# Optimization experiments

Measured on AMD Instinct MI355X. Metric: run time of the kernel, lower is better.

## Reference

```python
import jax, jax.numpy as jnp
import numpy as np
import math

H = 2048; NH = 16; HD = 128; E = 8; K = 2; F = 8192; CAP_F = 1.25
B = 2; S = 2048

def _layernorm(x, scale, bias, eps=1e-5):
    m = jnp.mean(x, axis=-1, keepdims=True)
    v = jnp.var(x, axis=-1, keepdims=True)
    return (x - m) * jax.lax.rsqrt(v + eps) * scale + bias

def _rope(x):
    # x: [B, S, NH, HD]; half-split RoPE, theta=10000
    hd = x.shape[-1]
    pos = jnp.arange(x.shape[1], dtype=jnp.float32)
    freqs = 1.0 / (10000.0 ** (jnp.arange(0, hd // 2, dtype=jnp.float32) / (hd // 2)))
    ang = pos[:, None] * freqs[None, :]              # [S, HD/2]
    cos = jnp.cos(ang)[None, :, None, :]
    sin = jnp.sin(ang)[None, :, None, :]
    x1, x2 = jnp.split(x, 2, axis=-1)
    return jnp.concatenate([x1 * cos - x2 * sin, x1 * sin + x2 * cos], axis=-1)

def setup_inputs() -> dict:
    key = jax.random.key(0)
    ks = jax.random.split(key, 16)
    std = 0.02
    inp = {
        'hidden_states': jax.random.normal(ks[0], (B, S, H), jnp.float32),
        'attention_mask': jnp.ones((B, S), jnp.int32),
        'ln1_scale': jnp.ones((H,), jnp.float32), 'ln1_bias': jnp.zeros((H,), jnp.float32),
        'ln2_scale': jnp.ones((H,), jnp.float32), 'ln2_bias': jnp.zeros((H,), jnp.float32),
        'Wq': jax.random.normal(ks[1], (H, NH * HD), jnp.float32) * std,
        'Wk': jax.random.normal(ks[2], (H, NH * HD), jnp.float32) * std,
        'Wv': jax.random.normal(ks[3], (H, NH * HD), jnp.float32) * std,
        'Wo': jax.random.normal(ks[4], (NH * HD, H), jnp.float32) * std,
        'Wg': jax.random.normal(ks[5], (H, H), jnp.float32) * std,
        'bg': jnp.zeros((H,), jnp.float32),
        'ls_attn': jnp.full((H,), 0.1, jnp.float32),
        'ls_moe': jnp.full((H,), 0.1, jnp.float32),
        'router_w': jax.random.normal(ks[6], (H, E), jnp.float32) * std,
        'W1': jax.random.normal(ks[7], (E, H, F), jnp.float32) * std,
        'b1': jnp.zeros((E, F), jnp.float32),
        'W2': jax.random.normal(ks[8], (E, F, H), jnp.float32) * std,
        'b2': jnp.zeros((E, H), jnp.float32),
    }
    return inp

def _forward(hidden_states, attention_mask, ln1_scale, ln1_bias, ln2_scale, ln2_bias,
             Wq, Wk, Wv, Wo, Wg, bg, ls_attn, ls_moe, router_w, W1, b1, W2, b2):
    b, s, h = hidden_states.shape
    # ---- pre-norm MLA attention + residual ----
    xn = _layernorm(hidden_states, ln1_scale, ln1_bias)
    q = (xn @ Wq).reshape(b, s, NH, HD)
    k = (xn @ Wk).reshape(b, s, NH, HD)
    v = (xn @ Wv).reshape(b, s, NH, HD)
    q = _rope(q); k = _rope(k)
    scores = jnp.einsum('bqhd,bkhd->bhqk', q, k) / math.sqrt(HD)
    causal = jnp.tril(jnp.ones((s, s), bool))
    mask = causal[None, None, :, :] & (attention_mask[:, None, None, :] > 0)
    scores = jnp.where(mask, scores, -1e9)
    attn = jax.nn.softmax(scores, axis=-1)
    ctx = jnp.einsum('bhqk,bkhd->bqhd', attn, v).reshape(b, s, NH * HD)
    attn_out = ctx @ Wo
    attn_out = attn_out * jax.nn.sigmoid(xn @ Wg + bg)   # output gating
    attn_out = attn_out * ls_attn                         # layer scale
    hidden_states = hidden_states + attn_out
    # ---- pre-norm MoE FFN + residual ----
    xn2 = _layernorm(hidden_states, ln2_scale, ln2_bias)
    T = b * s
    x = xn2.reshape(T, h)
    logits = (x @ router_w).astype(jnp.float32)           # [T, E]
    probs = jax.nn.softmax(logits, axis=-1)
    gates, idx = jax.lax.top_k(probs, K)                  # [T, K]
    gates = gates / jnp.sum(gates, axis=-1, keepdims=True)
    cap = int(math.ceil(T * K / E * CAP_F))               # expert capacity
    e_flat = idx.reshape(T * K)
    g_flat = gates.reshape(T * K)
    oh = jax.nn.one_hot(e_flat, E, dtype=jnp.int32)       # [TK, E]
    pos = jnp.sum(jnp.cumsum(oh, axis=0) * oh, axis=-1) - 1
    keep = (pos < cap).astype(x.dtype)
    pos_c = jnp.clip(pos, 0, cap - 1)
    x_rep = jnp.repeat(x, K, axis=0)                      # [TK, H]
    buf = jnp.zeros((E, cap, h), x.dtype).at[e_flat, pos_c].add(x_rep * keep[:, None])
    hmid = jax.nn.gelu(jnp.einsum('ech,ehf->ecf', buf, W1) + b1[:, None, :])
    obuf = jnp.einsum('ecf,efh->ech', hmid, W2) + b2[:, None, :]
    tok = obuf[e_flat, pos_c] * (keep * g_flat)[:, None]  # [TK, H]
    moe_out = tok.reshape(T, K, h).sum(axis=1).reshape(b, s, h)
    moe_out = moe_out * ls_moe
    return hidden_states + moe_out

def reference(hidden_states, attention_mask, ln1_scale, ln1_bias, ln2_scale, ln2_bias,
              Wq, Wk, Wv, Wo, Wg, bg, ls_attn, ls_moe, router_w, W1, b1, W2, b2):
    return _forward(hidden_states, attention_mask, ln1_scale, ln1_bias, ln2_scale, ln2_bias,
                    Wq, Wk, Wv, Wo, Wg, bg, ls_attn, ls_moe, router_w, W1, b1, W2, b2)
```

## Files before the change

kernel.cpp:

```cpp
#include <hip/hip_runtime.h>
#include <hip/hip_fp16.h>

typedef _Float16 f16;
typedef _Float16 half4 __attribute__((ext_vector_type(4)));
typedef _Float16 half8 __attribute__((ext_vector_type(8)));
typedef float floatx4 __attribute__((ext_vector_type(4)));

constexpr int kH  = 2048;
constexpr int kS  = 2048;
constexpr int kB  = 2;
constexpr int kT  = kB * kS;
constexpr int kNH = 16;
constexpr int kHD = 128;
constexpr int kE  = 8;
constexpr int kF  = 8192;
constexpr int kCAP = 1280;
constexpr int kTK = kT * 2;

__device__ __forceinline__ void gload16(const void* g, void* lds_) {
  __builtin_amdgcn_global_load_lds((const __attribute__((address_space(1))) void*)g,
                                   (__attribute__((address_space(3))) void*)lds_,
                                   16, 0, 0);
}

__device__ __forceinline__ void xcd_remap(int& bx, int& by, int& bz) {
  const int gx = gridDim.x, gy = gridDim.y;
  const int nwg = gx * gy * gridDim.z;
  int L = (bz * gy + by) * gx + bx;
  L = (L & 7) * (nwg >> 3) + (L >> 3);
  bz = L / (gx * gy);
  const int r = L - bz * gx * gy;
  by = r / gx;  bx = r - by * gx;
}

__global__ __launch_bounds__(256) void transpose_cvt(
    const float* __restrict__ src, f16* __restrict__ dst,
    int ldS, int ldD, long sZ, long dZ)
{
  __shared__ float tile[64][65];
  src += (long)blockIdx.z * sZ;
  dst += (long)blockIdx.z * dZ;
  const int kb = blockIdx.y * 64, nb = blockIdx.x * 64;
  const int tx = threadIdx.x & 15, ty = threadIdx.x >> 4;
#pragma unroll
  for (int i = 0; i < 4; i++) {
    const int r = ty + i * 16;
    const float4 v = *(const float4*)&src[(long)(kb + r) * ldS + nb + tx * 4];
    tile[r][tx * 4 + 0] = v.x; tile[r][tx * 4 + 1] = v.y;
    tile[r][tx * 4 + 2] = v.z; tile[r][tx * 4 + 3] = v.w;
  }
  __syncthreads();
  const int tx8 = threadIdx.x & 7, ty32 = threadIdx.x >> 3;
#pragma unroll
  for (int i = 0; i < 2; i++) {
    const int n = ty32 + i * 32;
    union { f16 h[8]; float4 v; } pk;
#pragma unroll
    for (int j = 0; j < 8; j++) pk.h[j] = (f16)tile[tx8 * 8 + j][n];
    *(float4*)&dst[(long)(nb + n) * ldD + kb + tx8 * 8] = pk.v;
  }
}

__global__ __launch_bounds__(256) void transpose_cvt5(
    const float* __restrict__ s0, const float* __restrict__ s1,
    const float* __restrict__ s2, const float* __restrict__ s3,
    const float* __restrict__ s4, f16* __restrict__ dst)
{
  __shared__ float tile[64][65];
  const float* src;
  switch (blockIdx.z) {
    case 0: src = s0; break;
    case 1: src = s1; break;
    case 2: src = s2; break;
    case 3: src = s3; break;
    default: src = s4; break;
  }
  dst += (long)blockIdx.z * kH * kH;
  const int kb = blockIdx.y * 64, nb = blockIdx.x * 64;
  const int tx = threadIdx.x & 15, ty = threadIdx.x >> 4;
#pragma unroll
  for (int i = 0; i < 4; i++) {
    const int r = ty + i * 16;
    const float4 v = *(const float4*)&src[(long)(kb + r) * kH + nb + tx * 4];
    tile[r][tx * 4 + 0] = v.x; tile[r][tx * 4 + 1] = v.y;
    tile[r][tx * 4 + 2] = v.z; tile[r][tx * 4 + 3] = v.w;
  }
  __syncthreads();
  const int tx8 = threadIdx.x & 7, ty32 = threadIdx.x >> 3;
#pragma unroll
  for (int i = 0; i < 2; i++) {
    const int n = ty32 + i * 32;
    union { f16 h[8]; float4 v; } pk;
#pragma unroll
    for (int j = 0; j < 8; j++) pk.h[j] = (f16)tile[tx8 * 8 + j][n];
    *(float4*)&dst[(long)(nb + n) * kH + kb + tx8 * 8] = pk.v;
  }
}

__global__ __launch_bounds__(256) void transpose_f16(
    const f16* __restrict__ src, f16* __restrict__ dst,
    int ldS, int ldD, long sZ, long dZ)
{
  __shared__ f16 tile[64][80];
  src += (long)blockIdx.z * sZ;
  dst += (long)blockIdx.z * dZ;
  const int kb = blockIdx.y * 64, nb = blockIdx.x * 64;
  const int tx = threadIdx.x & 7, ty = threadIdx.x >> 3;
#pragma unroll
  for (int i = 0; i < 2; i++) {
    const int r = ty + i * 32;
    *(half8*)&tile[r][tx * 8] =
        *(const half8*)&src[(long)(kb + r) * ldS + nb + tx * 8];
  }
  __syncthreads();
#pragma unroll
  for (int i = 0; i < 2; i++) {
    const int n = ty + i * 32;
    union { f16 h[8]; float4 v; } pk;
#pragma unroll
    for (int j = 0; j < 8; j++) pk.h[j] = tile[tx * 8 + j][n];
    *(float4*)&dst[(long)(nb + n) * ldD + kb + tx * 8] = pk.v;
  }
}

__global__ __launch_bounds__(256) void ln_kernel(
    const float* __restrict__ x, const float* __restrict__ sc,
    const float* __restrict__ bi, f16* __restrict__ o16, float* __restrict__ o32)
{
  const long row = blockIdx.x;
  const float* xr = x + row * kH;
  const int t = threadIdx.x;
  const float4 u = ((const float4*)xr)[t * 2];
  const float4 v = ((const float4*)xr)[t * 2 + 1];
  float s = u.x + u.y + u.z + u.w + v.x + v.y + v.z + v.w;
  float q = u.x*u.x + u.y*u.y + u.z*u.z + u.w*u.w + v.x*v.x + v.y*v.y + v.z*v.z + v.w*v.w;
#pragma unroll
  for (int m = 1; m < 64; m <<= 1) { s += __shfl_xor(s, m); q += __shfl_xor(q, m); }
  __shared__ float red_s[4], red_q[4];
  const int w = t >> 6, l = t & 63;
  if (l == 0) { red_s[w] = s; red_q[w] = q; }
  __syncthreads();
  s = red_s[0] + red_s[1] + red_s[2] + red_s[3];
  q = red_q[0] + red_q[1] + red_q[2] + red_q[3];
  const float mean = s * (1.f / kH);
  const float var = q * (1.f / kH) - mean * mean;
  const float rstd = rsqrtf(var + 1e-5f);
  const int c = t * 8;
  const float vals[8] = {u.x, u.y, u.z, u.w, v.x, v.y, v.z, v.w};
#pragma unroll
  for (int j = 0; j < 8; j++) {
    const float y = (vals[j] - mean) * rstd * sc[c + j] + bi[c + j];
    o16[row * kH + c + j] = (f16)y;
    if (o32 != nullptr) o32[row * kH + c + j] = y;
  }
}

#define STG(SRC, TILE, KC, PAR, MAT) { \
  const f16* s_ = (SRC) + (long)(TILE) * 64 + (KC) * 32; \
  char* d_ = lds + ((PAR) * 65536 + (MAT) * 32768 + (KC) * 16384) + ldsW; \
  gload16(s_, d_); \
  gload16(s_ + 128 * ldGl, d_ + 8192); }

#define MROW(MH, MM, AF) \
  acc[(MH)*4+(MM)][0] = __builtin_amdgcn_mfma_f32_16x16x32_f16(AF, bf0, acc[(MH)*4+(MM)][0], 0, 0, 0); \
  acc[(MH)*4+(MM)][1] = __builtin_amdgcn_mfma_f32_16x16x32_f16(AF, bf1, acc[(MH)*4+(MM)][1], 0, 0, 0); \
  acc[(MH)*4+(MM)][2] = __builtin_amdgcn_mfma_f32_16x16x32_f16(AF, bf2, acc[(MH)*4+(MM)][2], 0, 0, 0); \
  acc[(MH)*4+(MM)][3] = __builtin_amdgcn_mfma_f32_16x16x32_f16(AF, bf3, acc[(MH)*4+(MM)][3], 0, 0, 0);

#define PH(PAR, KC, MH, RB, STAGE_STMT, VM_STMT) { \
  const char* au_ = lds + ((PAR) * 65536 + (KC) * 16384); \
  const char* bu_ = lds + ((PAR) * 65536 + 32768 + (KC) * 16384); \
  af0 = *(const half8*)(au_ + afoff + (MH) * 4096 +    0); \
  af1 = *(const half8*)(au_ + afoff + (MH) * 4096 + 1024); \
  af2 = *(const half8*)(au_ + afoff + (MH) * 4096 + 2048); \
  af3 = *(const half8*)(au_ + afoff + (MH) * 4096 + 3072); \
  if (RB) { \
    bf0 = *(const half8*)(bu_ + bfoff +    0); \
    bf1 = *(const half8*)(bu_ + bfoff + 1024); \
    bf2 = *(const half8*)(bu_ + bfoff + 2048); \
    bf3 = *(const half8*)(bu_ + bfoff + 3072); \
  } \
  STAGE_STMT; \
  VM_STMT; \
  __builtin_amdgcn_sched_barrier(0); \
  __builtin_amdgcn_s_barrier(); \
  asm volatile("s_waitcnt lgkmcnt(0)" ::: "memory"); \
  __builtin_amdgcn_sched_barrier(0); \
  __builtin_amdgcn_s_setprio(1); \
  MROW(MH, 0, af0) MROW(MH, 1, af1) MROW(MH, 2, af2) MROW(MH, 3, af3) \
  __builtin_amdgcn_s_setprio(0); }

#define VM10 asm volatile("s_waitcnt vmcnt(10)" ::: "memory")
#define VM8  asm volatile("s_waitcnt vmcnt(8)" ::: "memory")
#define VM4  asm volatile("s_waitcnt vmcnt(4)" ::: "memory")
#define VM0  asm volatile("s_waitcnt vmcnt(0)" ::: "memory")
#define NOP (void)0

template <int EPI, int SK, bool XCD>
__global__ __launch_bounds__(512, 2) void gemm8p_kernel(
    const f16* __restrict__ A, const f16* __restrict__ B, void* __restrict__ Cv,
    const float* __restrict__ bias, const int* __restrict__ rowCount,
    int M, int N, int K, long ldA, long ldB, long aZ, long bZ, long cZ,
    long cZ2, long biasZ)
{
  int bx = blockIdx.x, by = blockIdx.y, bz = blockIdx.z;
  if (XCD) xcd_remap(bx, by, bz);
  const int z = bz;
  const int ze = z / SK;
  const int kq = z % SK;
  if (rowCount != nullptr && (int)(by * 256) >= rowCount[ze]) return;
  __shared__ __align__(16) char lds[131072];
  const long khoff = (long)kq * K;
  A += (long)ze * aZ + khoff;  B += (long)ze * bZ + khoff;
  const int tid = threadIdx.x, w = tid >> 6, l = tid & 63;
  const int g = l >> 4, lr = l & 15;
  const long m0 = (long)by * 256, n0 = (long)bx * 256;
  const int wm = (w >> 2) * 128, wn = (w & 3) * 64;

  floatx4 acc[8][4];
#pragma unroll
  for (int i = 0; i < 8; i++)
#pragma unroll
    for (int j = 0; j < 4; j++) acc[i][j] = floatx4{0.f, 0.f, 0.f, 0.f};

  const int swzS = ((l & 3) * 8) ^ (((l >> 3) & 3) << 3);
  const f16* aSrc;
  const f16* bSrc;
  long ldGl;
  {
    const int srow = w * 16 + (l >> 2);
    aSrc = A + (m0 + srow) * ldA + swzS;
    bSrc = B + (n0 + srow) * ldB + swzS;
  }
  ldGl = ldA;
  const int ldsW = w * 1024;
  const int rsw = (g * 16) ^ (((lr >> 1) & 3) << 4);
  const int afoff = wm * 64 + lr * 64 + rsw;
  const int bfoff = wn * 64 + lr * 64 + rsw;
  half8 af0, af1, af2, af3;
  half8 bf0 = half8{0}, bf1 = half8{0}, bf2 = half8{0}, bf3 = half8{0};

  STG(aSrc, 0, 0, 0, 0);
  STG(bSrc, 0, 0, 0, 1);
  STG(aSrc, 0, 1, 0, 0);
  STG(bSrc, 0, 1, 0, 1);
  STG(bSrc, 1, 0, 1, 1);
  STG(aSrc, 1, 0, 1, 0);
  STG(bSrc, 1, 1, 1, 1);
  VM10;
  __builtin_amdgcn_sched_barrier(0);
  __builtin_amdgcn_s_barrier();

  const int NI = K >> 7;
  for (int i = 0; i < NI - 1; i++) {
    const int t0 = 2 * i, t1 = 2 * i + 1;
    PH(0, 0, 0, 1, STG(aSrc, (t1),     1, 1, 0), VM10)
    PH(0, 0, 1, 0, STG(bSrc, (t0 + 2), 0, 0, 1), VM10)
    PH(0, 1, 0, 1, STG(aSrc, (t0 + 2), 0, 0, 0), VM10)
    PH(0, 1, 1, 0, STG(bSrc, (t0 + 2), 1, 0, 1), VM10)
    PH(1, 0, 0, 1, STG(aSrc, (t0 + 2), 1, 0, 0), VM10)
    PH(1, 0, 1, 0, STG(bSrc, (t1 + 2), 0, 1, 1), VM10)
    PH(1, 1, 0, 1, STG(aSrc, (t1 + 2), 0, 1, 0), VM10)
    PH(1, 1, 1, 0, STG(bSrc, (t1 + 2), 1, 1, 1), VM10)
  }
  {
    const int t1 = 2 * (NI - 1) + 1;
    PH(0, 0, 0, 1, STG(aSrc, (t1), 1, 1, 0), VM8)
    PH(0, 0, 1, 0, NOP, NOP)
    PH(0, 1, 0, 1, NOP, VM4)
    PH(0, 1, 1, 0, NOP, NOP)
    PH(1, 0, 0, 1, NOP, VM0)
    PH(1, 0, 1, 0, NOP, NOP)
    PH(1, 1, 0, 1, NOP, NOP)
    PH(1, 1, 1, 0, NOP, NOP)
  }

  const long crow = m0 + wm + g * 4;
  const long ccol = n0 + wn + lr;
  float* c32 = (float*)Cv + (long)ze * cZ + (long)kq * cZ2;
  f16* ch = (f16*)Cv + (long)ze * cZ + (long)kq * cZ2;
#pragma unroll
  for (int mi = 0; mi < 8; mi++)
#pragma unroll
    for (int ni = 0; ni < 4; ni++)
#pragma unroll
      for (int j = 0; j < 4; j++) {
        const long r = crow + mi * 16 + j;
        const long c = ccol + ni * 16;
        float v = acc[mi][ni][j];
        if (EPI == 0) {
          c32[r * N + c] = v;
        } else if (EPI == 2) {
          v += bias[(long)ze * biasZ + c];
          const float u2 = 1.5957691216057308f * (v + 0.044715f * v * v * v);
          const float sg = 1.f / (1.f + __expf(-u2));
          ((f16*)Cv)[(long)ze * cZ + r * N + c] = (f16)(v * sg);
        } else if (EPI == 3) {
          v += bias[(long)ze * biasZ + c];
          ((f16*)Cv)[(long)ze * cZ + r * N + c] = (f16)v;
        } else {
          ch[r * N + c] = (f16)v;
        }
      }
}
#undef STG
#undef MROW
#undef PH
#undef VM10
#undef VM8
#undef VM4
#undef VM0
#undef NOP

__global__ void rope_table_kernel(float* __restrict__ ct, float* __restrict__ st) {
  const int i = blockIdx.x * 256 + threadIdx.x;
  if (i >= kS * 64) return;
  const int s = i >> 6, f = i & 63;
  const double freq = exp(-0.14391156831212787 * (double)f);
  const double ang = (double)s * freq;
  ct[i] = (float)cos(ang);
  st[i] = (float)sin(ang);
}

__global__ __launch_bounds__(256) void rope_kernel(
    const f16* __restrict__ q, const f16* __restrict__ k,
    const float* __restrict__ ct, const float* __restrict__ st,
    f16* __restrict__ qr, f16* __restrict__ kr)
{
  const long t = blockIdx.x;
  const int s = (int)(t & (kS - 1)), b = (int)(t >> 11);
  for (int u = threadIdx.x; u < kNH * 64; u += 256) {
    const int h = u >> 6, i = u & 63;
    const float c = ct[s * 64 + i], sn = st[s * 64 + i];
    const long src = t * kH + h * kHD + i;
    const long dst = (((long)(b * kNH + h)) * kS + s) * kHD + i;
    float x1 = (float)q[src], x2 = (float)q[src + 64];
    qr[dst]      = (f16)((x1 * c - x2 * sn) * 0.08838834764831845f);
    qr[dst + 64] = (f16)((x1 * sn + x2 * c) * 0.08838834764831845f);
    x1 = (float)k[src]; x2 = (float)k[src + 64];
    kr[dst]      = (f16)(x1 * c - x2 * sn);
    kr[dst + 64] = (f16)(x1 * sn + x2 * c);
  }
}

__global__ __launch_bounds__(256) void attn_kernel(
    const f16* __restrict__ q_r, const f16* __restrict__ k_r,
    const f16* __restrict__ v_t, f16* __restrict__ ctx)
{
  __shared__ f16 Ks[64 * 128];
  __shared__ f16 Vs[128 * 64];
  __shared__ f16 Ps[4][1024];
  int qt = blockIdx.x, h = blockIdx.y, b = blockIdx.z;
  xcd_remap(qt, h, b);
  const int bh = b * kNH + h;
  const int tid = threadIdx.x, w = tid >> 6, l = tid & 63;
  const int g = l >> 4, lr = l & 15;
  const long q0 = (long)qt * 64;
  const f16* qbase = q_r + ((long)bh * kS + q0 + w * 16 + lr) * kHD;
  half8 qf[4];
#pragma unroll
  for (int kc = 0; kc < 4; kc++) qf[kc] = *(const half8*)(qbase + kc * 32 + g * 8);
  floatx4 acc[8];
#pragma unroll
  for (int i = 0; i < 8; i++) acc[i] = floatx4{0.f, 0.f, 0.f, 0.f};
  float mrun[4], lrun[4];
#pragma unroll
  for (int j = 0; j < 4; j++) { mrun[j] = -1e30f; lrun[j] = 0.f; }
  f16* pw = Ps[w];

  for (int kt = 0; kt <= qt; kt++) {
    const long k0 = (long)kt * 64;
#pragma unroll
    for (int c = 0; c < 4; c++) {
      const int cc = w * 4 + c;
      const int row = cc * 4 + (l >> 4);
      const int wb = (l & 15) * 16;
      const int src = (wb ^ ((row & 7) << 4)) >> 1;
      gload16(k_r + ((long)bh * kS + k0 + row) * kHD + src, Ks + cc * 512);
    }
#pragma unroll
    for (int c = 0; c < 4; c++) {
      const int cc = w * 4 + c;
      const int row = cc * 8 + (l >> 3);
      const int wb = (l & 7) * 16;
      const int src = (wb ^ ((row & 7) << 4)) >> 1;
      gload16(v_t + ((long)bh * kHD + row) * kS + k0 + src, Vs + cc * 512);
    }
    asm volatile("s_waitcnt vmcnt(0)" ::: "memory");
    __syncthreads();

    floatx4 sfr[4];
#pragma unroll
    for (int f = 0; f < 4; f++) {
      floatx4 s4 = floatx4{0.f, 0.f, 0.f, 0.f};
      const int row = f * 16 + lr;
#pragma unroll
      for (int kc = 0; kc < 4; kc++) {
        const half8 kfq = *(const half8*)((const char*)Ks + row * 256 +
                            ((kc * 64 + g * 16) ^ ((row & 7) << 4)));
        s4 = __builtin_amdgcn_mfma_f32_16x16x32_f16(qf[kc], kfq, s4, 0, 0, 0);
      }
      sfr[f] = s4;
    }
    if (kt == qt) {
#pragma unroll
      for (int f = 0; f < 4; f++) {
        const int key = kt * 64 + f * 16 + lr;
#pragma unroll
        for (int j = 0; j < 4; j++) {
          const int qrow = qt * 64 + w * 16 + g * 4 + j;
          if (key > qrow) sfr[f][j] = -1e30f;
        }
      }
    }
    float al[4];
#pragma unroll
    for (int j = 0; j < 4; j++) {
      float pm = fmaxf(fmaxf(sfr[0][j], sfr[1][j]), fmaxf(sfr[2][j], sfr[3][j]));
      pm = fmaxf(pm, __shfl_xor(pm, 1)); pm = fmaxf(pm, __shfl_xor(pm, 2));
      pm = fmaxf(pm, __shfl_xor(pm, 4)); pm = fmaxf(pm, __shfl_xor(pm, 8));
      const float mn = fmaxf(mrun[j], pm);
      al[j] = __expf(mrun[j] - mn);
      mrun[j] = mn;
      float rs = 0.f;
#pragma unroll
      for (int f = 0; f < 4; f++) {
        const float p = __expf(sfr[f][j] - mn);
        sfr[f][j] = p; rs += p;
      }
      rs += __shfl_xor(rs, 1); rs += __shfl_xor(rs, 2);
      rs += __shfl_xor(rs, 4); rs += __shfl_xor(rs, 8);
      lrun[j] = lrun[j] * al[j] + rs;
    }
#pragma unroll
    for (int nf = 0; nf < 8; nf++)
#pragma unroll
      for (int j = 0; j < 4; j++) acc[nf][j] *= al[j];
#pragma unroll
    for (int f = 0; f < 4; f++)
#pragma unroll
      for (int j = 0; j < 4; j++) {
        const int row = g * 4 + j;
        const int byteoff = (row * 128 + (f * 16 + lr) * 2) ^ ((row & 7) << 4);
        *(f16*)((char*)pw + byteoff) = (f16)sfr[f][j];
      }
#pragma unroll
    for (int kc = 0; kc < 2; kc++) {
      const half8 pf = *(const half8*)((const char*)pw + lr * 128 +
                         ((kc * 64 + g * 16) ^ ((lr & 7) << 4)));
#pragma unroll
      for (int nf = 0; nf < 8; nf++) {
        const int vrow = nf * 16 + lr;
        const half8 vfr = *(const half8*)((const char*)Vs + vrow * 128 +
                            ((kc * 64 + g * 16) ^ ((vrow & 7) << 4)));
        acc[nf] = __builtin_amdgcn_mfma_f32_16x16x32_f16(pf, vfr, acc[nf], 0, 0, 0);
      }
    }
    __syncthreads();
  }
  const long orow = (long)b * kS + q0 + w * 16;
#pragma unroll
  for (int j = 0; j < 4; j++) {
    const float inv = 1.0f / lrun[j];
    const int r = g * 4 + j;
#pragma unroll
    for (int nf = 0; nf < 8; nf++)
      ctx[(orow + r) * kH + h * kHD + nf * 16 + lr] = (f16)(acc[nf][j] * inv);
  }
}

__global__ __launch_bounds__(256) void combine1_kernel(
    const float* __restrict__ hid, const f16* __restrict__ a0,
    const f16* __restrict__ a1, const f16* __restrict__ glin,
    const float* __restrict__ bg, const float* __restrict__ ls,
    float* __restrict__ out)
{
  const long i = (long)blockIdx.x * 256 + threadIdx.x;
  const float4 hv = ((const float4*)hid)[i];
  const half4 av = ((const half4*)a0)[i];
  const half4 aw = ((const half4*)a1)[i];
  const half4 gv = ((const half4*)glin)[i];
  const int c = (int)(i & 511);
  const float4 lv = ((const float4*)ls)[c];
  const float4 bv = ((const float4*)bg)[c];
  float4 o;
  o.x = hv.x + lv.x * ((float)av[0] + (float)aw[0]) / (1.f + __expf(-((float)gv[0] + bv.x)));
  o.y = hv.y + lv.y * ((float)av[1] + (float)aw[1]) / (1.f + __expf(-((float)gv[1] + bv.y)));
  o.z = hv.z + lv.z * ((float)av[2] + (float)aw[2]) / (1.f + __expf(-((float)gv[2] + bv.z)));
  o.w = hv.w + lv.w * ((float)av[3] + (float)aw[3]) / (1.f + __expf(-((float)gv[3] + bv.w)));
  ((float4*)out)[i] = o;
}

__global__ __launch_bounds__(256) void router_kernel(
    const float* __restrict__ x, const float* __restrict__ rw,
    int* __restrict__ eidx, float* __restrict__ gates)
{
  const int t = blockIdx.x * 4 + (threadIdx.x >> 6);
  const int l = threadIdx.x & 63;
  const float* xr = x + (long)t * kH;
  float a[8] = {0.f, 0.f, 0.f, 0.f, 0.f, 0.f, 0.f, 0.f};
  for (int it = 0; it < kH / 64; it++) {
    const float xv = xr[it * 64 + l];
    const float* r = rw + (long)(it * 64 + l) * kE;
#pragma unroll
    for (int e = 0; e < 8; e++) a[e] += xv * r[e];
  }
#pragma unroll
  for (int e = 0; e < 8; e++)
#pragma unroll
    for (int m = 1; m < 64; m <<= 1) a[e] += __shfl_xor(a[e], m);
  if (l == 0) {
    float mx = a[0];
#pragma unroll
    for (int e = 1; e < 8; e++) mx = fmaxf(mx, a[e]);
    float p[8];
#pragma unroll
    for (int e = 0; e < 8; e++) p[e] = __expf(a[e] - mx);
    int i1 = 0; float v1 = p[0];
#pragma unroll
    for (int e = 1; e < 8; e++) if (p[e] > v1) { v1 = p[e]; i1 = e; }
    int i2 = -1; float v2 = -1.f;
#pragma unroll
    for (int e = 0; e < 8; e++) if (e != i1 && p[e] > v2) { v2 = p[e]; i2 = e; }
    const float inv = 1.f / (v1 + v2);
    eidx[t * 2] = i1; eidx[t * 2 + 1] = i2;
    gates[t * 2] = v1 * inv; gates[t * 2 + 1] = v2 * inv;
  }
}

__global__ void scan_kernel(const int* __restrict__ eidx, int* __restrict__ slot,
                            int* __restrict__ counts)
{
  const int l = threadIdx.x;
  int base[8] = {0, 0, 0, 0, 0, 0, 0, 0};
  const unsigned long long lt = (1ull << l) - 1ull;
  for (int it = 0; it < kTK / 64; it++) {
    const int i = it * 64 + l;
    const int e = eidx[i];
    int mypos = 0;
#pragma unroll
    for (int ex = 0; ex < 8; ex++) {
      const unsigned long long mk = __ballot(e == ex);
      if (e == ex) mypos = base[ex] + __popcll(mk & lt);
      base[ex] += __popcll(mk);
    }
    slot[i] = (mypos < kCAP) ? e * kCAP + mypos : -1;
  }
  if (l == 0) {
#pragma unroll
    for (int ex = 0; ex < 8; ex++) counts[ex] = min(base[ex], kCAP);
  }
}

__global__ __launch_bounds__(256) void scatter_kernel(
    const f16* __restrict__ xh, const int* __restrict__ slot, f16* __restrict__ buf)
{
  const int i = blockIdx.x;
  const int s = slot[i];
  if (s < 0) return;
  const long t = i >> 1;
  ((half8*)(buf + (long)s * kH))[threadIdx.x] =
      ((const half8*)(xh + t * kH))[threadIdx.x];
}

__global__ __launch_bounds__(256) void combine2_kernel(
    const float* __restrict__ hid2, const f16* __restrict__ P,
    const int* __restrict__ slot, const float* __restrict__ gates,
    const float* __restrict__ b2, const float* __restrict__ ls,
    float* __restrict__ out, long pS)
{
  const int t = blockIdx.x;
  const int c = threadIdx.x * 8;
  float m[8] = {0.f, 0.f, 0.f, 0.f, 0.f, 0.f, 0.f, 0.f};
#pragma unroll
  for (int ks = 0; ks < 2; ks++) {
    const int s = slot[t * 2 + ks];
    if (s < 0) continue;
    const float gte = gates[t * 2 + ks];
    const int e = s / kCAP;
    const long ro = (long)s * kH + c;
    float acc8[8];
    const float4 ba = *(const float4*)&b2[e * kH + c];
    const float4 bb = *(const float4*)&b2[e * kH + c + 4];
    acc8[0] = ba.x; acc8[1] = ba.y; acc8[2] = ba.z; acc8[3] = ba.w;
    acc8[4] = bb.x; acc8[5] = bb.y; acc8[6] = bb.z; acc8[7] = bb.w;
#pragma unroll
    for (int q = 0; q < 4; q++) {
      const half8 p = *(const half8*)&P[q * pS + ro];
#pragma unroll
      for (int j = 0; j < 8; j++) acc8[j] += (float)p[j];
    }
#pragma unroll
    for (int j = 0; j < 8; j++) m[j] += gte * acc8[j];
  }
  const float* hp = hid2 + (long)t * kH + c;
  float* op = out + (long)t * kH + c;
#pragma unroll
  for (int j = 0; j < 8; j++) op[j] = hp[j] + ls[c + j] * m[j];
}

extern "C" void kernel_launch(void* const* d_in, const int* in_sizes, int n_in,
                              void* d_out, int out_size, void* d_ws, size_t ws_size,
                              hipStream_t stream)
{
  (void)in_sizes; (void)n_in;
  const float* hidden   = (const float*)d_in[0];
  const float* ln1s     = (const float*)d_in[2];
  const float* ln1b     = (const float*)d_in[3];
  const float* ln2s     = (const float*)d_in[4];
  const float* ln2b     = (const float*)d_in[5];
  const float* Wq       = (const float*)d_in[6];
  const float* Wk       = (const float*)d_in[7];
  const float* Wv       = (const float*)d_in[8];
  const float* Wo       = (const float*)d_in[9];
  const float* Wg       = (const float*)d_in[10];
  const float* bg       = (const float*)d_in[11];
  const float* ls_attn  = (const float*)d_in[12];
  const float* ls_moe   = (const float*)d_in[13];
  const float* router_w = (const float*)d_in[14];
  const float* W1       = (const float*)d_in[15];
  const float* b1       = (const float*)d_in[16];
  const float* W2       = (const float*)d_in[17];
  const float* b2       = (const float*)d_in[18];

  char* ws = (char*)d_ws;
  size_t off = 0;
  auto take = [&](size_t b) { size_t r = off; off += (b + 255) & ~(size_t)255; return r; };
  const size_t o_wT   = take(5ULL * kH * kH * 2);
  const size_t o_w1t  = take((size_t)kE * kF * kH * 2);
  const size_t o_w2t  = take((size_t)kE * kH * kF * 2);
  const size_t o_xn   = take((size_t)kT * kH * 2);
  const size_t o_qkvg = take(4ULL * kT * kH * 4);
  const size_t o_tab  = take(2ULL * kS * 64 * 4);
  const size_t o_qr   = take(3ULL * kT * kH * 2);
  const size_t o_ctx  = take((size_t)kT * kH * 2);
  const size_t o_h2   = take((size_t)kT * kH * 4);
  const size_t o_sm   = take(1 << 20);
  const size_t o_hmid = take((size_t)kE * kCAP * kF * 2);
  if (off > ws_size) { hipMemsetAsync(d_out, 0xFF, (size_t)out_size * 4, stream); return; }

  f16* wT    = (f16*)(ws + o_wT);
  f16* w1t   = (f16*)(ws + o_w1t);
  f16* w2t   = (f16*)(ws + o_w2t);
  f16* xn    = (f16*)(ws + o_xn);
  float* tabc = (float*)(ws + o_tab);
  float* tabs = tabc + (size_t)kS * 64;
  f16* qr  = (f16*)(ws + o_qr);
  f16* kr  = qr + (size_t)kT * kH;
  f16* vt  = kr + (size_t)kT * kH;
  f16* ctx = (f16*)(ws + o_ctx);
  float* h2 = (float*)(ws + o_h2);
  int* eidx    = (int*)(ws + o_sm);
  float* gates = (float*)(ws + o_sm + 65536);
  int* slot    = (int*)(ws + o_sm + 131072);
  int* counts  = (int*)(ws + o_sm + 196608);
  f16* hmid = (f16*)(ws + o_hmid);

  const size_t S2 = (size_t)kT * kH * 2;
  char* R = ws + o_qkvg;
  f16* qh = (f16*)(R + 0 * S2);
  f16* kh = (f16*)(R + 1 * S2);
  f16* vh = (f16*)(R + 2 * S2);
  f16* gh = (f16*)(R + 3 * S2);
  float* x2f = (float*)(R + 4 * S2);
  f16* x2h   = (f16*)(R + 6 * S2);
  f16* woPh  = (f16*)(R + 0 * S2);
  f16* buf  = qr;
  f16* Ph = (f16*)(ws + o_w1t);
  const long pS = (long)kE * kCAP * kH;

  const long HH = (long)kH * kH;

  ln_kernel<<<kT, 256, 0, stream>>>(hidden, ln1s, ln1b, xn, nullptr);
  transpose_cvt5<<<dim3(32, 32, 5), 256, 0, stream>>>(Wq, Wk, Wv, Wg, Wo, wT);
  gemm8p_kernel<4, 1, true><<<dim3(kH / 256, kT / 256, 4), 512, 0, stream>>>(
      xn, wT, qh, nullptr, nullptr, kT, kH, kH, kH, kH,
      0L, HH, (long)kT * kH, 0L, 0L);
  rope_table_kernel<<<(kS * 64 + 255) / 256, 256, 0, stream>>>(tabc, tabs);
  rope_kernel<<<kT, 256, 0, stream>>>(qh, kh, tabc, tabs, qr, kr);
  for (int b = 0; b < kB; b++)
    transpose_f16<<<dim3(kHD / 64, kS / 64, kNH), 256, 0, stream>>>(
        vh + (size_t)b * kS * kH, vt + (size_t)b * kNH * kHD * kS,
        kH, kS, 128L, (long)kHD * kS);
  attn_kernel<<<dim3(kS / 64, kNH, kB), 256, 0, stream>>>(qr, kr, vt, ctx);
  gemm8p_kernel<4, 2, true><<<dim3(kH / 256, kT / 256, 2), 512, 0, stream>>>(
      ctx, wT + 4 * HH, woPh, nullptr, nullptr, kT, kH, 1024, kH, kH,
      0L, 0L, 0L, (long)kT * kH, 0L);
  combine1_kernel<<<(kT * kH / 4) / 256, 256, 0, stream>>>(
      hidden, woPh, woPh + (size_t)kT * kH, gh, bg, ls_attn, h2);
  ln_kernel<<<kT, 256, 0, stream>>>(h2, ln2s, ln2b, x2h, x2f);
  router_kernel<<<kT / 4, 256, 0, stream>>>(x2f, router_w, eidx, gates);
  scan_kernel<<<1, 64, 0, stream>>>(eidx, slot, counts);
  scatter_kernel<<<kTK, 256, 0, stream>>>(x2h, slot, buf);
  transpose_cvt<<<dim3(kF / 64, kH / 64, kE), 256, 0, stream>>>(
      W1, w1t, kF, kH, (long)kH * kF, (long)kF * kH);
  gemm8p_kernel<2, 1, false><<<dim3(kF / 256, kCAP / 256, kE), 512, 0, stream>>>(
      buf, w1t, hmid, b1, counts, kCAP, kF, kH, kH, kH,
      (long)kCAP * kH, (long)kF * kH, (long)kCAP * kF, 0L, (long)kF);
  transpose_cvt<<<dim3(kH / 64, kF / 64, kE), 256, 0, stream>>>(
      W2, w2t, kH, kF, (long)kF * kH, (long)kH * kF);
  gemm8p_kernel<4, 4, false><<<dim3(kH / 256, kCAP / 256, 4 * kE), 512, 0, stream>>>(
      hmid, w2t, Ph, nullptr, counts, kCAP, kH, 2048, kF, kF,
      (long)kCAP * kF, (long)kH * kF, (long)kCAP * kH, pS, 0L);
  combine2_kernel<<<kT, 256, 0, stream>>>(
      h2, Ph, slot, gates, b2, ls_moe, (float*)d_out, pS);
}
```

Baseline: 1.520 ms.

## Shrink GEMM tiles to 128x128 with 4-wave blocks and retuned pipeline

Replaces the 256x256, 8-wave GEMM with a 128x128, 4-wave variant. It halves LDS use, reschedules the double-buffered 64-wide K loop with new vmcnt waits, and quadruples the grid size. This gives finer row-count skipping for the MoE capacity buffers and more blocks per CU, at the cost of lower per-block data reuse. It also uses a raw v_rcp in the GELU epilogue and raises wave priority around the attention MFMA sections.

```diff
diff --git a/kernel.cpp b/kernel.cpp
--- a/kernel.cpp
+++ b/kernel.cpp
@@ -157,23 +157,21 @@
 
 #define STG(SRC, TILE, KC, PAR, MAT) { \
   const f16* s_ = (SRC) + (long)(TILE) * 64 + (KC) * 32; \
-  char* d_ = lds + ((PAR) * 65536 + (MAT) * 32768 + (KC) * 16384) + ldsW; \
+  char* d_ = lds + ((PAR) * 32768 + (MAT) * 16384 + (KC) * 8192) + ldsW; \
   gload16(s_, d_); \
-  gload16(s_ + 128 * ldGl, d_ + 8192); }
-
-#define MROW(MH, MM, AF) \
-  acc[(MH)*4+(MM)][0] = __builtin_amdgcn_mfma_f32_16x16x32_f16(AF, bf0, acc[(MH)*4+(MM)][0], 0, 0, 0); \
-  acc[(MH)*4+(MM)][1] = __builtin_amdgcn_mfma_f32_16x16x32_f16(AF, bf1, acc[(MH)*4+(MM)][1], 0, 0, 0); \
-  acc[(MH)*4+(MM)][2] = __builtin_amdgcn_mfma_f32_16x16x32_f16(AF, bf2, acc[(MH)*4+(MM)][2], 0, 0, 0); \
-  acc[(MH)*4+(MM)][3] = __builtin_amdgcn_mfma_f32_16x16x32_f16(AF, bf3, acc[(MH)*4+(MM)][3], 0, 0, 0);
+  gload16(s_ + 64 * ldGl, d_ + 4096); }
+
+#define MROW(RI, AF) \
+  acc[(RI)][0] = __builtin_amdgcn_mfma_f32_16x16x32_f16(AF, bf0, acc[(RI)][0], 0, 0, 0); \
+  acc[(RI)][1] = __builtin_amdgcn_mfma_f32_16x16x32_f16(AF, bf1, acc[(RI)][1], 0, 0, 0); \
+  acc[(RI)][2] = __builtin_amdgcn_mfma_f32_16x16x32_f16(AF, bf2, acc[(RI)][2], 0, 0, 0); \
+  acc[(RI)][3] = __builtin_amdgcn_mfma_f32_16x16x32_f16(AF, bf3, acc[(RI)][3], 0, 0, 0);
 
 #define PH(PAR, KC, MH, RB, STAGE_STMT, VM_STMT) { \
-  const char* au_ = lds + ((PAR) * 65536 + (KC) * 16384); \
-  const char* bu_ = lds + ((PAR) * 65536 + 32768 + (KC) * 16384); \
-  af0 = *(const half8*)(au_ + afoff + (MH) * 4096 +    0); \
-  af1 = *(const half8*)(au_ + afoff + (MH) * 4096 + 1024); \
-  af2 = *(const half8*)(au_ + afoff + (MH) * 4096 + 2048); \
-  af3 = *(const half8*)(au_ + afoff + (MH) * 4096 + 3072); \
+  const char* au_ = lds + ((PAR) * 32768 + (KC) * 8192); \
+  const char* bu_ = lds + ((PAR) * 32768 + 16384 + (KC) * 8192); \
+  af0 = *(const half8*)(au_ + afoff + (MH) * 2048 +    0); \
+  af1 = *(const half8*)(au_ + afoff + (MH) * 2048 + 1024); \
   if (RB) { \
     bf0 = *(const half8*)(bu_ + bfoff +    0); \
     bf1 = *(const half8*)(bu_ + bfoff + 1024); \
@@ -187,7 +185,7 @@
   asm volatile("s_waitcnt lgkmcnt(0)" ::: "memory"); \
   __builtin_amdgcn_sched_barrier(0); \
   __builtin_amdgcn_s_setprio(1); \
-  MROW(MH, 0, af0) MROW(MH, 1, af1) MROW(MH, 2, af2) MROW(MH, 3, af3) \
+  MROW((MH) * 2 + 0, af0) MROW((MH) * 2 + 1, af1) \
   __builtin_amdgcn_s_setprio(0); }
 
 #define VM10 asm volatile("s_waitcnt vmcnt(10)" ::: "memory")
@@ -197,7 +195,7 @@
 #define NOP (void)0
 
 template <int EPI, int SK, bool XCD>
-__global__ __launch_bounds__(512, 2) void gemm8p_kernel(
+__global__ __launch_bounds__(256, 2) void gemm4w_kernel(
     const f16* __restrict__ A, const f16* __restrict__ B, void* __restrict__ Cv,
     const float* __restrict__ bias, const int* __restrict__ rowCount,
     int M, int N, int K, long ldA, long ldB, long aZ, long bZ, long cZ,
@@ -208,18 +206,18 @@
   const int z = bz;
   const int ze = z / SK;
   const int kq = z % SK;
-  if (rowCount != nullptr && (int)(by * 256) >= rowCount[ze]) return;
-  __shared__ __align__(16) char lds[131072];
+  if (rowCount != nullptr && (int)(by * 128) >= rowCount[ze]) return;
+  __shared__ __align__(16) char lds[65536];
   const long khoff = (long)kq * K;
   A += (long)ze * aZ + khoff;  B += (long)ze * bZ + khoff;
   const int tid = threadIdx.x, w = tid >> 6, l = tid & 63;
   const int g = l >> 4, lr = l & 15;
-  const long m0 = (long)by * 256, n0 = (long)bx * 256;
-  const int wm = (w >> 2) * 128, wn = (w & 3) * 64;
-
-  floatx4 acc[8][4];
-#pragma unroll
-  for (int i = 0; i < 8; i++)
+  const long m0 = (long)by * 128, n0 = (long)bx * 128;
+  const int wm = (w >> 1) * 64, wn = (w & 1) * 64;
+
+  floatx4 acc[4][4];
+#pragma unroll
+  for (int i = 0; i < 4; i++)
 #pragma unroll
     for (int j = 0; j < 4; j++) acc[i][j] = floatx4{0.f, 0.f, 0.f, 0.f};
 
@@ -237,42 +235,41 @@
   const int rsw = (g * 16) ^ (((lr >> 1) & 3) << 4);
   const int afoff = wm * 64 + lr * 64 + rsw;
   const int bfoff = wn * 64 + lr * 64 + rsw;
-  half8 af0, af1, af2, af3;
+  half8 af0, af1;
   half8 bf0 = half8{0}, bf1 = half8{0}, bf2 = half8{0}, bf3 = half8{0};
 
   STG(aSrc, 0, 0, 0, 0);
   STG(bSrc, 0, 0, 0, 1);
   STG(aSrc, 0, 1, 0, 0);
   STG(bSrc, 0, 1, 0, 1);
+  STG(aSrc, 1, 0, 1, 0);
   STG(bSrc, 1, 0, 1, 1);
-  STG(aSrc, 1, 0, 1, 0);
-  STG(bSrc, 1, 1, 1, 1);
+  STG(aSrc, 1, 1, 1, 0);
   VM10;
   __builtin_amdgcn_sched_barrier(0);
   __builtin_amdgcn_s_barrier();
 
-  const int NI = K >> 7;
-  for (int i = 0; i < NI - 1; i++) {
-    const int t0 = 2 * i, t1 = 2 * i + 1;
-    PH(0, 0, 0, 1, STG(aSrc, (t1),     1, 1, 0), VM10)
-    PH(0, 0, 1, 0, STG(bSrc, (t0 + 2), 0, 0, 1), VM10)
-    PH(0, 1, 0, 1, STG(aSrc, (t0 + 2), 0, 0, 0), VM10)
-    PH(0, 1, 1, 0, STG(bSrc, (t0 + 2), 1, 0, 1), VM10)
-    PH(1, 0, 0, 1, STG(aSrc, (t0 + 2), 1, 0, 0), VM10)
-    PH(1, 0, 1, 0, STG(bSrc, (t1 + 2), 0, 1, 1), VM10)
-    PH(1, 1, 0, 1, STG(aSrc, (t1 + 2), 0, 1, 0), VM10)
-    PH(1, 1, 1, 0, STG(bSrc, (t1 + 2), 1, 1, 1), VM10)
+  const int NT = K >> 6;
+  for (int t = 0; t < NT - 2; t++) {
+    const int p = t & 1;
+    PH(p, 0, 0, 1, STG(bSrc, (t + 1), 1, p ^ 1, 1), NOP)
+    PH(p, 0, 1, 0, STG(aSrc, (t + 2), 0, p,     0), VM10)
+    PH(p, 1, 0, 1, STG(bSrc, (t + 2), 0, p,     1), NOP)
+    PH(p, 1, 1, 0, STG(aSrc, (t + 2), 1, p,     0), VM10)
   }
   {
-    const int t1 = 2 * (NI - 1) + 1;
-    PH(0, 0, 0, 1, STG(aSrc, (t1), 1, 1, 0), VM8)
-    PH(0, 0, 1, 0, NOP, NOP)
-    PH(0, 1, 0, 1, NOP, VM4)
-    PH(0, 1, 1, 0, NOP, NOP)
-    PH(1, 0, 0, 1, NOP, VM0)
-    PH(1, 0, 1, 0, NOP, NOP)
-    PH(1, 1, 0, 1, NOP, NOP)
-    PH(1, 1, 1, 0, NOP, NOP)
+    const int t = NT - 2, p = t & 1;
+    PH(p, 0, 0, 1, STG(bSrc, (t + 1), 1, p ^ 1, 1), NOP)
+    PH(p, 0, 1, 0, NOP, VM8)
+    PH(p, 1, 0, 1, NOP, NOP)
+    PH(p, 1, 1, 0, NOP, VM4)
+  }
+  {
+    const int p = (NT - 1) & 1;
+    PH(p, 0, 0, 1, NOP, NOP)
+    PH(p, 0, 1, 0, NOP, VM0)
+    PH(p, 1, 0, 1, NOP, NOP)
+    PH(p, 1, 1, 0, NOP, NOP)
   }
 
   const long crow = m0 + wm + g * 4;
@@ -280,7 +277,7 @@
   float* c32 = (float*)Cv + (long)ze * cZ + (long)kq * cZ2;
   f16* ch = (f16*)Cv + (long)ze * cZ + (long)kq * cZ2;
 #pragma unroll
-  for (int mi = 0; mi < 8; mi++)
+  for (int mi = 0; mi < 4; mi++)
 #pragma unroll
     for (int ni = 0; ni < 4; ni++)
 #pragma unroll
@@ -293,7 +290,9 @@
         } else if (EPI == 2) {
           v += bias[(long)ze * biasZ + c];
           const float u2 = 1.5957691216057308f * (v + 0.044715f * v * v * v);
-          const float sg = 1.f / (1.f + __expf(-u2));
+          const float den = 1.f + __expf(-u2);
+          float sg;
+          asm("v_rcp_f32 %0, %1" : "=v"(sg) : "v"(den));
           ((f16*)Cv)[(long)ze * cZ + r * N + c] = (f16)(v * sg);
         } else if (EPI == 3) {
           v += bias[(long)ze * biasZ + c];
@@ -390,6 +389,7 @@
     __syncthreads();
 
     floatx4 sfr[4];
+    __builtin_amdgcn_s_setprio(1);
 #pragma unroll
     for (int f = 0; f < 4; f++) {
       floatx4 s4 = floatx4{0.f, 0.f, 0.f, 0.f};
@@ -402,6 +402,7 @@
       }
       sfr[f] = s4;
     }
+    __builtin_amdgcn_s_setprio(0);
     if (kt == qt) {
 #pragma unroll
       for (int f = 0; f < 4; f++) {
@@ -444,6 +445,7 @@
         const int byteoff = (row * 128 + (f * 16 + lr) * 2) ^ ((row & 7) << 4);
         *(f16*)((char*)pw + byteoff) = (f16)sfr[f][j];
       }
+    __builtin_amdgcn_s_setprio(1);
 #pragma unroll
     for (int kc = 0; kc < 2; kc++) {
       const half8 pf = *(const half8*)((const char*)pw + lr * 128 +
@@ -456,6 +458,7 @@
         acc[nf] = __builtin_amdgcn_mfma_f32_16x16x32_f16(pf, vfr, acc[nf], 0, 0, 0);
       }
     }
+    __builtin_amdgcn_s_setprio(0);
     __syncthreads();
   }
   const long orow = (long)b * kS + q0 + w * 16;
@@ -673,7 +676,7 @@
 
   ln_kernel<<<kT, 256, 0, stream>>>(hidden, ln1s, ln1b, xn, nullptr);
   transpose_cvt5<<<dim3(32, 32, 5), 256, 0, stream>>>(Wq, Wk, Wv, Wg, Wo, wT);
-  gemm8p_kernel<4, 1, true><<<dim3(kH / 256, kT / 256, 4), 512, 0, stream>>>(
+  gemm4w_kernel<4, 1, true><<<dim3(kH / 128, kT / 128, 4), 256, 0, stream>>>(
       xn, wT, qh, nullptr, nullptr, kT, kH, kH, kH, kH,
       0L, HH, (long)kT * kH, 0L, 0L);
   rope_table_kernel<<<(kS * 64 + 255) / 256, 256, 0, stream>>>(tabc, tabs);
@@ -683,7 +686,7 @@
         vh + (size_t)b * kS * kH, vt + (size_t)b * kNH * kHD * kS,
         kH, kS, 128L, (long)kHD * kS);
   attn_kernel<<<dim3(kS / 64, kNH, kB), 256, 0, stream>>>(qr, kr, vt, ctx);
-  gemm8p_kernel<4, 2, true><<<dim3(kH / 256, kT / 256, 2), 512, 0, stream>>>(
+  gemm4w_kernel<4, 2, true><<<dim3(kH / 128, kT / 128, 2), 256, 0, stream>>>(
       ctx, wT + 4 * HH, woPh, nullptr, nullptr, kT, kH, 1024, kH, kH,
       0L, 0L, 0L, (long)kT * kH, 0L);
   combine1_kernel<<<(kT * kH / 4) / 256, 256, 0, stream>>>(
@@ -694,12 +697,12 @@
   scatter_kernel<<<kTK, 256, 0, stream>>>(x2h, slot, buf);
   transpose_cvt<<<dim3(kF / 64, kH / 64, kE), 256, 0, stream>>>(
       W1, w1t, kF, kH, (long)kH * kF, (long)kF * kH);
-  gemm8p_kernel<2, 1, false><<<dim3(kF / 256, kCAP / 256, kE), 512, 0, stream>>>(
+  gemm4w_kernel<2, 1, false><<<dim3(kF / 128, kCAP / 128, kE), 256, 0, stream>>>(
       buf, w1t, hmid, b1, counts, kCAP, kF, kH, kH, kH,
       (long)kCAP * kH, (long)kF * kH, (long)kCAP * kF, 0L, (long)kF);
   transpose_cvt<<<dim3(kH / 64, kF / 64, kE), 256, 0, stream>>>(
       W2, w2t, kH, kF, (long)kF * kH, (long)kH * kF);
-  gemm8p_kernel<4, 4, false><<<dim3(kH / 256, kCAP / 256, 4 * kE), 512, 0, stream>>>(
+  gemm4w_kernel<4, 4, false><<<dim3(kH / 128, kCAP / 128, 4 * kE), 256, 0, stream>>>(
       hmid, w2t, Ph, nullptr, counts, kCAP, kH, 2048, kF, kF,
       (long)kCAP * kF, (long)kH * kF, (long)kCAP * kH, pS, 0L);
   combine2_kernel<<<kT, 256, 0, stream>>>(
```

Result: slower. 1.639 ms (+7.9%).
